# Kernel tuning notes

Hardware: AMD Instinct MI355X
Metric: run time of the kernel (lower is better)

Reference implementation:

```python
import jax, jax.numpy as jnp
import numpy as np

IMAGE_SIZE = 288.0
LAMBDA_NOOBJ = 0.5
LAMBDA_COOR = 5.0
_ANCHOR_DIMS = np.array([[0.24, 0.24], [0.12, 0.12], [0.08, 0.08], [0.28, 0.28], [0.15, 0.15]], np.float32)
ANCHORS = jnp.concatenate([jnp.full((5, 2), 0.5, jnp.float32), jnp.asarray(_ANCHOR_DIMS)], axis=1)  # [cx,cy,w,h]


def _corners(box):
    # matches torch _format_bbox column order used in _get_iou: (x1, x2, y1, y2)
    cx, cy, w, h = box[..., 0], box[..., 1], box[..., 2], box[..., 3]
    return cx - w / 2, cx + w / 2, cy - h / 2, cy + h / 2


def _iou(b1, b2):
    x1a, x2a, y1a, y2a = _corners(b1)
    x1b, x2b, y1b, y2b = _corners(b2)
    iw = jnp.minimum(x2a, x2b) - jnp.maximum(x1a, x1b) + 1.0
    ih = jnp.minimum(y2a, y2b) - jnp.maximum(y1a, y1b) + 1.0
    inter = iw * ih
    a1 = (x2a - x1a + 1.0) * (y2a - y1a + 1.0)
    a2 = (x2b - x1b + 1.0) * (y2b - y1b + 1.0)
    return inter / (a1 + a2 - inter + 1e-16)


def setup_inputs() -> dict:
    key = jax.random.key(0)
    k1, k2, k3, k4 = jax.random.split(key, 4)
    B, G, A, T = 32, 36, 5, 8
    return {
        "bbox_prediction": jax.random.normal(k1, (B, G, G, A, 5), jnp.float32),
        "landmarks_prediction": jax.random.normal(k2, (B, G, G, A, 68, 2), jnp.float32),
        "bbox_target": jax.random.uniform(k3, (B, T, 4), jnp.float32),
        "landmarks_target": jax.random.uniform(k4, (B, T, 68, 2), jnp.float32),
    }


def _forward(bbox_prediction, landmarks_prediction, bbox_target, landmarks_target):
    B, G, _, A, _ = bbox_prediction.shape
    T = bbox_target.shape[1]
    N = B * G * G * A

    valid = bbox_target.sum(-1) != 0  # (B,T)
    gx = bbox_target[..., 0] * G
    gy = bbox_target[..., 1] * G
    gi = jnp.floor(gx).astype(jnp.int32)  # int(gt_x)
    gj = jnp.floor(gy).astype(jnp.int32)
    fx = gx - gi
    fy = gy - gj
    gt_anchor_box = jnp.stack([fx, fy, bbox_target[..., 2], bbox_target[..., 3]], -1)  # (B,T,4)

    # vectorized anchor assignment (replaces per-target python loop)
    anchor_iou = _iou(gt_anchor_box[:, :, None, :], ANCHORS[None, None, :, :])  # (B,T,A)
    best_a = jnp.argmax(anchor_iou, -1).astype(jnp.int32)
    log_box = jnp.log1p(gt_anchor_box)  # (B,T,4) -- torch stores log1p form

    lin = ((jnp.arange(B)[:, None] * G + gj) * G + gi) * A + best_a  # (B,T) flat (b,j,i,a)
    lin = jnp.where(valid, lin, N)  # invalid targets -> dump slot N

    obj = jnp.zeros(N + 1, jnp.float32).at[lin.ravel()].set(1.0)[:N].reshape(B, G, G, A)
    noobj = 1.0 - obj

    t_ids = jnp.broadcast_to(jnp.arange(T, dtype=jnp.int32), (B, T))
    seg_last = jax.ops.segment_max(t_ids.ravel(), lin.ravel(), num_segments=N + 1)
    winner = (seg_last[lin] == t_ids) & valid
    lin_w = jnp.where(winner, lin, N).ravel()

    gt_boxes = jnp.zeros((N + 1, 4), jnp.float32).at[lin_w].set(log_box.reshape(-1, 4))[:N].reshape(B, G, G, A, 4)
    gt_lm = jnp.zeros((N + 1, 136), jnp.float32).at[lin_w].set(landmarks_target.reshape(B * T, 136))[:N].reshape(B, G, G, A, 136)

    nobj = jnp.maximum(obj.sum(), 1.0)

    # NME over object cells (masked-mean expressed as weighted sum -> static shapes)
    diff = landmarks_prediction.reshape(B, G, G, A, 136) - gt_lm
    dist = jnp.sqrt(jnp.sum(diff * diff, -1))  # (B,G,G,A)
    wh = gt_boxes[..., 2] * gt_boxes[..., 3]  # note: log1p(w)*log1p(h), as in torch
    norm = jnp.sqrt(jnp.where(obj > 0, wh, 1.0)) * IMAGE_SIZE * 68.0 * nobj
    nme = jnp.sum(obj * dist / norm)

    # localization: SmoothL1 (beta=1), mean over masked elements
    d = bbox_prediction[..., :4] - gt_boxes
    ad = jnp.abs(d)
    sl1 = jnp.where(ad < 1.0, 0.5 * d * d, ad - 0.5)
    loc_loss = LAMBDA_COOR * jnp.sum(obj[..., None] * sl1) / (nobj * 4.0)

    # confidence: MSE on noobj (target 0) + MSE on obj (target 1)
    conf_pred = bbox_prediction[..., 4]
    n_noobj = jnp.maximum(noobj.sum(), 1.0)
    conf_loss = LAMBDA_NOOBJ * jnp.sum(noobj * conf_pred ** 2) / n_noobj + jnp.sum(obj * (conf_pred - 1.0) ** 2) / nobj

    # best predicted bbox per target (IoU of log1p gt box vs raw cell predictions, as in torch)
    cell_pred = bbox_prediction[jnp.arange(B)[:, None], gj, gi]  # (B,T,A,5)
    pred_iou = _iou(log_box[:, :, None, :], cell_pred[..., :4])  # (B,T,A)
    best_p = jnp.argmax(pred_iou, -1)
    best = jnp.take_along_axis(cell_pred, best_p[..., None, None], axis=2)[:, :, 0]  # (B,T,5)
    x1, x2, y1, y2 = _corners(best[..., :4])
    best_pred = jnp.where(valid[..., None], jnp.stack([x1, x2, y1, y2, best[..., 4]], -1), 0.0)

    return nme, loc_loss, conf_loss, best_pred


def reference(bbox_prediction, landmarks_prediction, bbox_target, landmarks_target):
    return _forward(bbox_prediction, landmarks_prediction, bbox_target, landmarks_target)
```

## Files before the change

kernel.cpp:

```cpp
#include <hip/hip_runtime.h>
#include <math.h>

#define Gc 36
#define Ac 5
#define Bc 32
#define Tc 8
#define NCELLS (Bc*Gc*Gc*Ac)
#define NT 256
#define NBLK1 256

__global__ void conf_sq_partial(const float* __restrict__ bbox_pred,
                                float* __restrict__ partial) {
    __shared__ float red[NT];
    float acc = 0.0f;
    for (int idx = blockIdx.x * blockDim.x + threadIdx.x; idx < NCELLS;
         idx += gridDim.x * blockDim.x) {
        float c = bbox_pred[(size_t)idx * 5 + 4];
        acc += c * c;
    }
    red[threadIdx.x] = acc;
    __syncthreads();
    for (int s = NT / 2; s > 0; s >>= 1) {
        if (threadIdx.x < s) red[threadIdx.x] += red[threadIdx.x + s];
        __syncthreads();
    }
    if (threadIdx.x == 0) partial[blockIdx.x] = red[0];
}

__device__ __forceinline__ float block_sum(float v, float* red, int tid) {
    red[tid] = v;
    __syncthreads();
    for (int s = NT / 2; s > 0; s >>= 1) {
        if (tid < s) red[tid] += red[tid + s];
        __syncthreads();
    }
    float r = red[0];
    __syncthreads();
    return r;
}

__global__ void finalize(const float* __restrict__ bbox_pred,
                         const float* __restrict__ lm_pred,
                         const float* __restrict__ bbox_tgt,
                         const float* __restrict__ lm_tgt,
                         const float* __restrict__ partial,
                         float* __restrict__ out) {
    const int tid = threadIdx.x;
    const int b = tid >> 3;
    const int t = tid & 7;

    __shared__ int   s_lin[NT];
    __shared__ float s_red[NT];
    __shared__ int   s_cnt[NT];

    const float* tg = bbox_tgt + (size_t)(b * Tc + t) * 4;
    float x = tg[0], y = tg[1], w = tg[2], h = tg[3];
    bool valid = ((x + y + w + h) != 0.0f);

    float gx = x * (float)Gc, gy = y * (float)Gc;
    int gi = (int)floorf(gx);
    int gj = (int)floorf(gy);
    float fx = gx - (float)gi;
    float fy = gy - (float)gj;

    float x1a = fx - w * 0.5f, x2a = fx + w * 0.5f;
    float y1a = fy - h * 0.5f, y2a = fy + h * 0.5f;
    float a1 = (x2a - x1a + 1.0f) * (y2a - y1a + 1.0f);

    const float adim[Ac] = {0.24f, 0.12f, 0.08f, 0.28f, 0.15f};
    int best_a = 0;
    float best_iou = -1e30f;
    for (int a = 0; a < Ac; ++a) {
        float x1b = 0.5f - adim[a] * 0.5f, x2b = 0.5f + adim[a] * 0.5f;
        float y1b = x1b, y2b = x2b;
        float iw = fminf(x2a, x2b) - fmaxf(x1a, x1b) + 1.0f;
        float ih = fminf(y2a, y2b) - fmaxf(y1a, y1b) + 1.0f;
        float inter = iw * ih;
        float a2 = (x2b - x1b + 1.0f) * (y2b - y1b + 1.0f);
        float iou = inter / (a1 + a2 - inter + 1e-16f);
        if (iou > best_iou) { best_iou = iou; best_a = a; }
    }

    float l0 = log1pf(fx), l1 = log1pf(fy), l2 = log1pf(w), l3 = log1pf(h);

    int lin = valid ? (((b * Gc + gj) * Gc + gi) * Ac + best_a) : NCELLS;
    s_lin[tid] = lin;
    __syncthreads();

    bool winner = valid;
    if (valid) {
        for (int t2 = t + 1; t2 < Tc; ++t2) {
            if (s_lin[(b << 3) + t2] == lin) { winner = false; break; }
        }
    }

    float c_nme = 0.0f, c_sl1 = 0.0f, c_cobj = 0.0f, c_csq = 0.0f;
    int c_cnt = 0;
    if (winner) {
        c_cnt = 1;
        const float* bp = bbox_pred + (size_t)lin * 5;
        float conf = bp[4];
        c_cobj = (conf - 1.0f) * (conf - 1.0f);
        c_csq  = conf * conf;
        float lb[4] = {l0, l1, l2, l3};
        for (int k = 0; k < 4; ++k) {
            float d = bp[k] - lb[k];
            float ad = fabsf(d);
            c_sl1 += (ad < 1.0f) ? 0.5f * d * d : (ad - 0.5f);
        }
        const float* lp = lm_pred + (size_t)lin * 136;
        const float* lt = lm_tgt + (size_t)(b * Tc + t) * 136;
        float acc = 0.0f;
        for (int j = 0; j < 136; ++j) {
            float d = lp[j] - lt[j];
            acc += d * d;
        }
        float dist = sqrtf(acc);
        float wh = l2 * l3;
        c_nme = dist / (sqrtf(wh) * 288.0f * 68.0f);
    }

    s_cnt[tid] = c_cnt;
    __syncthreads();
    for (int s = NT / 2; s > 0; s >>= 1) {
        if (tid < s) s_cnt[tid] += s_cnt[tid + s];
        __syncthreads();
    }
    int cnt = s_cnt[0];
    __syncthreads();

    float nobj    = fmaxf((float)cnt, 1.0f);
    float n_noobj = fmaxf((float)(NCELLS - cnt), 1.0f);

    float sum_nme  = block_sum(c_nme,  s_red, tid);
    float sum_sl1  = block_sum(c_sl1,  s_red, tid);
    float sum_cobj = block_sum(c_cobj, s_red, tid);
    float sum_csq  = block_sum(c_csq,  s_red, tid);
    float s_total  = block_sum(partial[tid], s_red, tid);

    if (tid == 0) {
        out[0] = sum_nme / nobj;
        out[1] = 5.0f * sum_sl1 / (nobj * 4.0f);
        out[2] = 0.5f * (s_total - sum_csq) / n_noobj
               + sum_cobj / nobj;
    }

    const float* cp = bbox_pred + (size_t)((b * Gc + gj) * Gc + gi) * Ac * 5;
    float x1g = l0 - l2 * 0.5f, x2g = l0 + l2 * 0.5f;
    float y1g = l1 - l3 * 0.5f, y2g = l1 + l3 * 0.5f;
    float ag = (x2g - x1g + 1.0f) * (y2g - y1g + 1.0f);
    int bp_idx = 0;
    float bp_iou = -1e30f;
    for (int a = 0; a < Ac; ++a) {
        float cx = cp[a * 5 + 0], cy = cp[a * 5 + 1];
        float pw = cp[a * 5 + 2], ph = cp[a * 5 + 3];
        float x1p = cx - pw * 0.5f, x2p = cx + pw * 0.5f;
        float y1p = cy - ph * 0.5f, y2p = cy + ph * 0.5f;
        float iw = fminf(x2g, x2p) - fmaxf(x1g, x1p) + 1.0f;
        float ih = fminf(y2g, y2p) - fmaxf(y1g, y1p) + 1.0f;
        float inter = iw * ih;
        float ap = (x2p - x1p + 1.0f) * (y2p - y1p + 1.0f);
        float iou = inter / (ag + ap - inter + 1e-16f);
        if (iou > bp_iou) { bp_iou = iou; bp_idx = a; }
    }
    float bx = cp[bp_idx * 5 + 0], by = cp[bp_idx * 5 + 1];
    float bw = cp[bp_idx * 5 + 2], bh = cp[bp_idx * 5 + 3];
    float bconf = cp[bp_idx * 5 + 4];
    float o0 = bx - bw * 0.5f, o1 = bx + bw * 0.5f;
    float o2 = by - bh * 0.5f, o3 = by + bh * 0.5f;

    float* op = out + 3 + (size_t)tid * 5;
    if (valid) {
        op[0] = o0; op[1] = o1; op[2] = o2; op[3] = o3; op[4] = bconf;
    } else {
        op[0] = 0.0f; op[1] = 0.0f; op[2] = 0.0f; op[3] = 0.0f; op[4] = 0.0f;
    }
}

extern "C" void kernel_launch(void* const* d_in, const int* in_sizes, int n_in,
                              void* d_out, int out_size, void* d_ws, size_t ws_size,
                              hipStream_t stream) {
    const float* bbox_pred = (const float*)d_in[0];
    const float* lm_pred   = (const float*)d_in[1];
    const float* bbox_tgt  = (const float*)d_in[2];
    const float* lm_tgt    = (const float*)d_in[3];
    float* out = (float*)d_out;
    float* partial = (float*)d_ws;

    conf_sq_partial<<<NBLK1, NT, 0, stream>>>(bbox_pred, partial);
    finalize<<<1, NT, 0, stream>>>(bbox_pred, lm_pred, bbox_tgt, lm_tgt,
                                   partial, out);
}
```

Before: 172.1 us.

## Split landmark distance into parallel per-target kernel and vectorize conf reduction

Moves the 136-element landmark squared-distance loop out of the single-block finalize kernel into its own kernel with one 64-lane block per target. That kernel uses float4 loads and a wavefront shuffle reduction. The confidence sum-of-squares pass now reads bbox_pred as float4 and picks out the conf lane by index modulo 5. Target assignment and winner detection run in an extra block of the first kernel. This removes the serial per-thread gather in the one-block tail at the cost of a third kernel launch and workspace round-trips.

```diff
diff --git a/kernel.cpp b/kernel.cpp
--- a/kernel.cpp
+++ b/kernel.cpp
@@ -6,121 +6,154 @@
 #define Bc 32
 #define Tc 8
 #define NCELLS (Bc*Gc*Gc*Ac)
+#define NFLOATS (NCELLS*5)
+#define NF4 (NFLOATS/4)
 #define NT 256
-#define NBLK1 256
-
-__global__ void conf_sq_partial(const float* __restrict__ bbox_pred,
-                                float* __restrict__ partial) {
-    __shared__ float red[NT];
-    float acc = 0.0f;
-    for (int idx = blockIdx.x * blockDim.x + threadIdx.x; idx < NCELLS;
-         idx += gridDim.x * blockDim.x) {
-        float c = bbox_pred[(size_t)idx * 5 + 4];
-        acc += c * c;
-    }
-    red[threadIdx.x] = acc;
-    __syncthreads();
-    for (int s = NT / 2; s > 0; s >>= 1) {
-        if (threadIdx.x < s) red[threadIdx.x] += red[threadIdx.x + s];
-        __syncthreads();
-    }
-    if (threadIdx.x == 0) partial[blockIdx.x] = red[0];
-}
-
-__device__ __forceinline__ float block_sum(float v, float* red, int tid) {
-    red[tid] = v;
-    __syncthreads();
-    for (int s = NT / 2; s > 0; s >>= 1) {
-        if (tid < s) red[tid] += red[tid + s];
-        __syncthreads();
-    }
-    float r = red[0];
-    __syncthreads();
-    return r;
-}
-
-__global__ void finalize(const float* __restrict__ bbox_pred,
-                         const float* __restrict__ lm_pred,
-                         const float* __restrict__ bbox_tgt,
-                         const float* __restrict__ lm_tgt,
-                         const float* __restrict__ partial,
-                         float* __restrict__ out) {
-    const int tid = threadIdx.x;
-    const int b = tid >> 3;
-    const int t = tid & 7;
-
-    __shared__ int   s_lin[NT];
-    __shared__ float s_red[NT];
-    __shared__ int   s_cnt[NT];
-
+#define CONF_BLOCKS 128
+
+
+__device__ __forceinline__ void target_meta(const float* __restrict__ bbox_tgt,
+                                            int tid, bool& valid, int& gi, int& gj,
+                                            float& fx, float& fy, float& w, float& h,
+                                            int& best_a) {
+    const int b = tid >> 3, t = tid & 7;
     const float* tg = bbox_tgt + (size_t)(b * Tc + t) * 4;
-    float x = tg[0], y = tg[1], w = tg[2], h = tg[3];
-    bool valid = ((x + y + w + h) != 0.0f);
-
+    float x = tg[0], y = tg[1];
+    w = tg[2]; h = tg[3];
+    valid = ((x + y + w + h) != 0.0f);
     float gx = x * (float)Gc, gy = y * (float)Gc;
-    int gi = (int)floorf(gx);
-    int gj = (int)floorf(gy);
-    float fx = gx - (float)gi;
-    float fy = gy - (float)gj;
+    gi = (int)floorf(gx); gj = (int)floorf(gy);
+    gi = min(max(gi, 0), Gc - 1); gj = min(max(gj, 0), Gc - 1);
+    fx = gx - floorf(gx); fy = gy - floorf(gy);
 
     float x1a = fx - w * 0.5f, x2a = fx + w * 0.5f;
     float y1a = fy - h * 0.5f, y2a = fy + h * 0.5f;
     float a1 = (x2a - x1a + 1.0f) * (y2a - y1a + 1.0f);
-
     const float adim[Ac] = {0.24f, 0.12f, 0.08f, 0.28f, 0.15f};
-    int best_a = 0;
+    best_a = 0;
     float best_iou = -1e30f;
     for (int a = 0; a < Ac; ++a) {
         float x1b = 0.5f - adim[a] * 0.5f, x2b = 0.5f + adim[a] * 0.5f;
-        float y1b = x1b, y2b = x2b;
         float iw = fminf(x2a, x2b) - fmaxf(x1a, x1b) + 1.0f;
-        float ih = fminf(y2a, y2b) - fmaxf(y1a, y1b) + 1.0f;
+        float ih = fminf(y2a, x2b) - fmaxf(y1a, x1b) + 1.0f;
         float inter = iw * ih;
-        float a2 = (x2b - x1b + 1.0f) * (y2b - y1b + 1.0f);
+        float a2 = (x2b - x1b + 1.0f) * (x2b - x1b + 1.0f);
         float iou = inter / (a1 + a2 - inter + 1e-16f);
         if (iou > best_iou) { best_iou = iou; best_a = a; }
     }
+}
+
+__global__ __launch_bounds__(NT) void k1_conf_meta(
+        const float* __restrict__ bbox_pred,
+        const float* __restrict__ bbox_tgt,
+        float* __restrict__ ws_f, int* __restrict__ ws_i) {
+    if (blockIdx.x < CONF_BLOCKS) {
+        __shared__ float red[NT];
+        const float4* p4 = (const float4*)bbox_pred;
+        float acc = 0.0f;
+        for (int j = blockIdx.x * NT + threadIdx.x; j < NF4;
+             j += CONF_BLOCKS * NT) {
+            float4 f = p4[j];
+            int r = (4 * j) % 5;
+            float v = (r == 4) ? f.x : (r == 3) ? f.y : (r == 2) ? f.z
+                    : (r == 1) ? f.w : 0.0f;
+            acc += v * v;
+        }
+        red[threadIdx.x] = acc;
+        __syncthreads();
+        for (int s = NT / 2; s > 0; s >>= 1) {
+            if (threadIdx.x < s) red[threadIdx.x] += red[threadIdx.x + s];
+            __syncthreads();
+        }
+        if (threadIdx.x == 0) ws_f[blockIdx.x] = red[0];
+    } else {
+        __shared__ int s_lin[NT];
+        const int tid = threadIdx.x;
+        const int b = tid >> 3, t = tid & 7;
+        bool valid; int gi, gj, best_a; float fx, fy, w, h;
+        target_meta(bbox_tgt, tid, valid, gi, gj, fx, fy, w, h, best_a);
+        int lin = valid ? (((b * Gc + gj) * Gc + gi) * Ac + best_a) : NCELLS;
+        s_lin[tid] = lin;
+        __syncthreads();
+        bool winner = valid;
+        if (valid) {
+            for (int t2 = t + 1; t2 < Tc; ++t2)
+                if (s_lin[(b << 3) + t2] == lin) { winner = false; break; }
+        }
+        ws_i[256 + tid] = lin;
+        ws_i[512 + tid] = winner ? 1 : 0;
+    }
+}
+
+__global__ __launch_bounds__(64) void k2_lmdist(
+        const float* __restrict__ lm_pred,
+        const float* __restrict__ lm_tgt,
+        const int* __restrict__ ws_i,
+        float* __restrict__ ws_f) {
+    const int tgt = blockIdx.x;
+    const int lane = threadIdx.x;
+    int winner = ws_i[512 + tgt];
+    int lin = ws_i[256 + tgt];
+    float acc = 0.0f;
+    if (winner && lane < 34) {
+        const float4* lp = (const float4*)(lm_pred + (size_t)lin * 136);
+        const float4* lt = (const float4*)(lm_tgt + (size_t)tgt * 136);
+        float4 a = lp[lane], b = lt[lane];
+        float dx = a.x - b.x, dy = a.y - b.y, dz = a.z - b.z, dw = a.w - b.w;
+        acc = dx * dx + dy * dy + dz * dz + dw * dw;
+    }
+    for (int off = 32; off > 0; off >>= 1)
+        acc += __shfl_down(acc, off, 64);
+    if (lane == 0) ws_f[1024 + tgt] = winner ? sqrtf(acc) : 0.0f;
+}
+
+__device__ __forceinline__ float block_sum(float v, float* red, int tid) {
+    red[tid] = v;
+    __syncthreads();
+    for (int s = NT / 2; s > 0; s >>= 1) {
+        if (tid < s) red[tid] += red[tid + s];
+        __syncthreads();
+    }
+    float r = red[0];
+    __syncthreads();
+    return r;
+}
+
+__global__ __launch_bounds__(NT) void k3_final(
+        const float* __restrict__ bbox_pred,
+        const float* __restrict__ bbox_tgt,
+        const float* __restrict__ ws_f,
+        const int* __restrict__ ws_i,
+        float* __restrict__ out) {
+    const int tid = threadIdx.x;
+    const int b = tid >> 3, t = tid & 7;
+    __shared__ float s_red[NT];
+    __shared__ int s_cnt[NT];
+
+    bool valid; int gi, gj, best_a; float fx, fy, w, h;
+    target_meta(bbox_tgt, tid, valid, gi, gj, fx, fy, w, h, best_a);
+    int lin = ws_i[256 + tid];
+    int winner = ws_i[512 + tid];
+    float dist = ws_f[1024 + tid];
 
     float l0 = log1pf(fx), l1 = log1pf(fy), l2 = log1pf(w), l3 = log1pf(h);
 
-    int lin = valid ? (((b * Gc + gj) * Gc + gi) * Ac + best_a) : NCELLS;
-    s_lin[tid] = lin;
-    __syncthreads();
-
-    bool winner = valid;
-    if (valid) {
-        for (int t2 = t + 1; t2 < Tc; ++t2) {
-            if (s_lin[(b << 3) + t2] == lin) { winner = false; break; }
-        }
-    }
-
     float c_nme = 0.0f, c_sl1 = 0.0f, c_cobj = 0.0f, c_csq = 0.0f;
-    int c_cnt = 0;
     if (winner) {
-        c_cnt = 1;
         const float* bp = bbox_pred + (size_t)lin * 5;
         float conf = bp[4];
         c_cobj = (conf - 1.0f) * (conf - 1.0f);
-        c_csq  = conf * conf;
+        c_csq = conf * conf;
         float lb[4] = {l0, l1, l2, l3};
         for (int k = 0; k < 4; ++k) {
             float d = bp[k] - lb[k];
             float ad = fabsf(d);
             c_sl1 += (ad < 1.0f) ? 0.5f * d * d : (ad - 0.5f);
         }
-        const float* lp = lm_pred + (size_t)lin * 136;
-        const float* lt = lm_tgt + (size_t)(b * Tc + t) * 136;
-        float acc = 0.0f;
-        for (int j = 0; j < 136; ++j) {
-            float d = lp[j] - lt[j];
-            acc += d * d;
-        }
-        float dist = sqrtf(acc);
-        float wh = l2 * l3;
-        c_nme = dist / (sqrtf(wh) * 288.0f * 68.0f);
-    }
-
-    s_cnt[tid] = c_cnt;
+        c_nme = dist / (sqrtf(l2 * l3) * 288.0f * 68.0f);
+    }
+
+    s_cnt[tid] = winner;
     __syncthreads();
     for (int s = NT / 2; s > 0; s >>= 1) {
         if (tid < s) s_cnt[tid] += s_cnt[tid + s];
@@ -128,21 +161,19 @@
     }
     int cnt = s_cnt[0];
     __syncthreads();
-
-    float nobj    = fmaxf((float)cnt, 1.0f);
+    float nobj = fmaxf((float)cnt, 1.0f);
     float n_noobj = fmaxf((float)(NCELLS - cnt), 1.0f);
 
-    float sum_nme  = block_sum(c_nme,  s_red, tid);
-    float sum_sl1  = block_sum(c_sl1,  s_red, tid);
+    float sum_nme  = block_sum(c_nme, s_red, tid);
+    float sum_sl1  = block_sum(c_sl1, s_red, tid);
     float sum_cobj = block_sum(c_cobj, s_red, tid);
-    float sum_csq  = block_sum(c_csq,  s_red, tid);
-    float s_total  = block_sum(partial[tid], s_red, tid);
+    float sum_csq  = block_sum(c_csq, s_red, tid);
+    float s_total  = block_sum(tid < CONF_BLOCKS ? ws_f[tid] : 0.0f, s_red, tid);
 
     if (tid == 0) {
         out[0] = sum_nme / nobj;
         out[1] = 5.0f * sum_sl1 / (nobj * 4.0f);
-        out[2] = 0.5f * (s_total - sum_csq) / n_noobj
-               + sum_cobj / nobj;
+        out[2] = 0.5f * (s_total - sum_csq) / n_noobj + sum_cobj / nobj;
     }
 
     const float* cp = bbox_pred + (size_t)((b * Gc + gj) * Gc + gi) * Ac * 5;
@@ -166,12 +197,10 @@
     float bx = cp[bp_idx * 5 + 0], by = cp[bp_idx * 5 + 1];
     float bw = cp[bp_idx * 5 + 2], bh = cp[bp_idx * 5 + 3];
     float bconf = cp[bp_idx * 5 + 4];
-    float o0 = bx - bw * 0.5f, o1 = bx + bw * 0.5f;
-    float o2 = by - bh * 0.5f, o3 = by + bh * 0.5f;
-
     float* op = out + 3 + (size_t)tid * 5;
     if (valid) {
-        op[0] = o0; op[1] = o1; op[2] = o2; op[3] = o3; op[4] = bconf;
+        op[0] = bx - bw * 0.5f; op[1] = bx + bw * 0.5f;
+        op[2] = by - bh * 0.5f; op[3] = by + bh * 0.5f; op[4] = bconf;
     } else {
         op[0] = 0.0f; op[1] = 0.0f; op[2] = 0.0f; op[3] = 0.0f; op[4] = 0.0f;
     }
@@ -185,9 +214,10 @@
     const float* bbox_tgt  = (const float*)d_in[2];
     const float* lm_tgt    = (const float*)d_in[3];
     float* out = (float*)d_out;
-    float* partial = (float*)d_ws;
-
-    conf_sq_partial<<<NBLK1, NT, 0, stream>>>(bbox_pred, partial);
-    finalize<<<1, NT, 0, stream>>>(bbox_pred, lm_pred, bbox_tgt, lm_tgt,
-                                   partial, out);
-}
+    float* ws_f = (float*)d_ws;
+    int* ws_i = (int*)d_ws;
+
+    k1_conf_meta<<<CONF_BLOCKS + 1, NT, 0, stream>>>(bbox_pred, bbox_tgt, ws_f, ws_i);
+    k2_lmdist<<<256, 64, 0, stream>>>(lm_pred, lm_tgt, ws_i, ws_f);
+    k3_final<<<1, NT, 0, stream>>>(bbox_pred, bbox_tgt, ws_f, ws_i, out);
+}
```

Measured after the change: 159.0 us. -7.6%, faster.
